# Kernel tuning notes

Measured on AMD Instinct MI355X. Metric: run time of the kernel, lower is better.

The kernel has to match this reference:

```python
import jax, jax.numpy as jnp
import numpy as np
import math

B, H, W, DM = 4, 64, 64, 96
DS, DCONV, EXPAND = 16, 3, 2
DI = EXPAND * DM
DTR = math.ceil(DM / 16)
K = 4
HID = 4 * DI


def layernorm(x, g, b, eps=1e-5):
    m = x.mean(-1, keepdims=True)
    v = ((x - m) ** 2).mean(-1, keepdims=True)
    return (x - m) / jnp.sqrt(v + eps) * g + b


def dwconv(x, w, b=None):
    # x: (B,C,H,W), w: (C,1,kh,kw) depthwise, odd kernel => SAME padding == k//2
    out = jax.lax.conv_general_dilated(x, w, (1, 1), 'SAME',
                                       feature_group_count=x.shape[1],
                                       dimension_numbers=('NCHW', 'OIHW', 'NCHW'))
    if b is not None:
        out = out + b[None, :, None, None]
    return out


def ss2d_core(xc, x_proj_w, dt_projs_w, dt_projs_b, A_logs, Ds):
    # xc: (b, d_inner, h, w) -> (b, d_inner, L) summed over 4 scan directions
    b, c, h, w = xc.shape
    L = h * w
    x_hw = xc.reshape(b, c, L)
    x_wh = xc.transpose(0, 1, 3, 2).reshape(b, c, L)
    xs = jnp.stack([x_hw, x_wh], axis=1)                 # (b,2,c,L)
    xs = jnp.concatenate([xs, jnp.flip(xs, -1)], axis=1)  # (b,4,c,L)
    x_dbl = jnp.einsum('bkdl,kcd->bkcl', xs, x_proj_w)
    dts, Bs, Cs = jnp.split(x_dbl, [DTR, DTR + DS], axis=2)
    dts = jnp.einsum('bkrl,kdr->bkdl', dts, dt_projs_w)
    delta = jax.nn.softplus(dts + dt_projs_b[None, :, :, None])  # (b,K,c,L)
    A = -jnp.exp(A_logs).reshape(K, c, DS)                       # (K,c,n)

    def step(hst, inp):
        x_t, d_t, B_t, C_t = inp  # (b,K,c),(b,K,c),(b,K,n),(b,K,n)
        dA = jnp.exp(d_t[..., None] * A)                       # (b,K,c,n)
        hst = hst * dA + (d_t * x_t)[..., None] * B_t[:, :, None, :]
        y = jnp.einsum('bkdn,bkn->bkd', hst, C_t)
        return hst, y

    seq = (jnp.moveaxis(xs, -1, 0), jnp.moveaxis(delta, -1, 0),
           jnp.moveaxis(Bs, -1, 0), jnp.moveaxis(Cs, -1, 0))
    h0 = jnp.zeros((b, K, c, DS), xc.dtype)
    _, ys = jax.lax.scan(step, h0, seq)          # (L,b,K,c)
    ys = jnp.moveaxis(ys, 0, -1)                 # (b,K,c,L)
    ys = ys + Ds.reshape(K, c)[None, :, :, None] * xs
    y1 = ys[:, 0]
    inv = jnp.flip(ys[:, 2:4], -1)
    y2 = inv[:, 0]
    wh = ys[:, 1].reshape(b, c, w, h).swapaxes(2, 3).reshape(b, c, L)
    invwh = inv[:, 1].reshape(b, c, w, h).swapaxes(2, 3).reshape(b, c, L)
    return y1 + y2 + wh + invwh


def msffn(y, in_w, in_b, dw1, dw3, dw5, ln_g, ln_b, out_w, out_b):
    hcl = jax.nn.silu(y @ in_w.T + in_b)          # (b,h,w,HID)
    hc = hcl.transpose(0, 3, 1, 2)
    hc = hc + dwconv(hc, dw1) + dwconv(hc, dw3) + dwconv(hc, dw5)
    hn = layernorm(hc.transpose(0, 2, 3, 1), ln_g, ln_b)
    return hn @ out_w.T + out_b


def setup_inputs() -> dict:
    key = jax.random.key(0)
    ks = jax.random.split(key, 16)
    dt_init_std = DTR ** -0.5
    dt = jnp.exp(jax.random.uniform(ks[0], (K, DI)) * (math.log(0.1) - math.log(0.001)) + math.log(0.001))
    dt = jnp.clip(dt, 1e-4, None)
    inv_dt = dt + jnp.log(-jnp.expm1(-dt))          # softplus-inverse init for dt bias
    A_logs = jnp.tile(jnp.log(jnp.arange(1, DS + 1, dtype=jnp.float32))[None, :], (K * DI, 1))
    r = lambda i, sh, s: jax.random.normal(ks[i], sh, jnp.float32) * s
    return {
        'x': r(1, (B, H, W, DM), 1.0),
        'in_proj_w': r(2, (2 * DI, DM), DM ** -0.5),
        'conv_w': r(3, (DI, 1, DCONV, DCONV), 0.2),
        'conv_b': jnp.zeros((DI,), jnp.float32),
        'x_proj_w': r(4, (K, DTR + 2 * DS, DI), DI ** -0.5),
        'dt_projs_w': jax.random.uniform(ks[5], (K, DI, DTR), minval=-dt_init_std, maxval=dt_init_std),
        'dt_projs_b': inv_dt,
        'A_logs': A_logs,
        'Ds': jnp.ones((K * DI,), jnp.float32),
        'out_norm_g': jnp.ones((DI,), jnp.float32),
        'out_norm_b': jnp.zeros((DI,), jnp.float32),
        'out_proj_w': r(6, (DM, DI), DI ** -0.5),
        'ffn_in_w': r(7, (HID, DI), DI ** -0.5),
        'ffn_in_b': jnp.zeros((HID,), jnp.float32),
        'ffn_dw1': r(8, (HID, 1, 1, 1), 0.3),
        'ffn_dw3': r(9, (HID, 1, 3, 3), 0.2),
        'ffn_dw5': r(10, (HID, 1, 5, 5), 0.1),
        'ffn_ln_g': jnp.ones((HID,), jnp.float32),
        'ffn_ln_b': jnp.zeros((HID,), jnp.float32),
        'ffn_out_w': r(11, (DM, HID), HID ** -0.5),
        'ffn_out_b': jnp.zeros((DM,), jnp.float32),
        'skip_scale': jnp.ones((1,), jnp.float32),
    }


def reference(x, in_proj_w, conv_w, conv_b, x_proj_w, dt_projs_w, dt_projs_b, A_logs, Ds,
              out_norm_g, out_norm_b, out_proj_w, ffn_in_w, ffn_in_b, ffn_dw1, ffn_dw3,
              ffn_dw5, ffn_ln_g, ffn_ln_b, ffn_out_w, ffn_out_b, skip_scale):
    b, h, w, _ = x.shape
    xz = x @ in_proj_w.T                          # (b,h,w,2*DI)
    xi, z = jnp.split(xz, 2, axis=-1)
    xc = jax.nn.silu(dwconv(xi.transpose(0, 3, 1, 2), conv_w, conv_b))  # (b,DI,h,w)
    y = ss2d_core(xc, x_proj_w, dt_projs_w, dt_projs_b, A_logs, Ds)     # (b,DI,L)
    y = y.swapaxes(1, 2).reshape(b, h, w, DI)
    y = layernorm(y, out_norm_g, out_norm_b)
    y = y * jax.nn.silu(z)
    out = y @ out_proj_w.T
    ffn = msffn(y, ffn_in_w, ffn_in_b, ffn_dw1, ffn_dw3, ffn_dw5,
                ffn_ln_g, ffn_ln_b, ffn_out_w, ffn_out_b)
    return out + skip_scale * ffn
```

## Files before the change

kernel.cpp:

```cpp
#include <hip/hip_runtime.h>
#include <hip/hip_bf16.h>

constexpr int BB = 4, HH = 64, WW = 64, DMv = 96;
constexpr int DSn = 16, DIv = 192, DTRv = 6, KKv = 4, HIDv = 768;
constexpr int LL = 4096;
constexpr int NC = 32, CHK = LL / NC;
constexpr int NR = BB * LL;
constexpr int XDS = 40;

constexpr size_t S_xi   = (size_t)BB * LL * DIv;
constexpr size_t S_xdbl = (size_t)BB * KKv * LL * XDS;
constexpr size_t S_big  = (size_t)BB * KKv * LL * DIv;
constexpr size_t S_sp   = (size_t)BB * KKv * NC * DIv * DSn;

typedef __attribute__((ext_vector_type(8))) short short8;
typedef __attribute__((ext_vector_type(4))) short short4v;
typedef __attribute__((ext_vector_type(4))) float floatx4;

__device__ __forceinline__ float sigf(float x) { return 1.f / (1.f + __expf(-x)); }
__device__ __forceinline__ float softp(float x) {
  return (x > 20.f) ? x : __logf(1.f + __expf(x));
}
__device__ __forceinline__ short bfbits(float v) {
  __hip_bfloat16 h = __float2bfloat16(v);
  return *(short*)&h;
}

__device__ __forceinline__ int lmap(int k, int l) {
  int lr = (k & 2) ? (LL - 1 - l) : l;
  return (k & 1) ? (((lr & 63) << 6) | (lr >> 6)) : lr;
}

__global__ void k_wprep(const float* __restrict__ fiw, const float* __restrict__ opw,
                        const float* __restrict__ fow, const float* __restrict__ in_w,
                        const float* __restrict__ xpw, const float* __restrict__ x,
                        float* __restrict__ wt, float* __restrict__ wcatT,
                        float* __restrict__ xt, short* __restrict__ fiwP,
                        short* __restrict__ opwP, short* __restrict__ fowP) {
  int bx = blockIdx.x, t = threadIdx.x;
  __shared__ float smbuf[32 * 65];
  if (bx < 36) {
    int r0 = (bx / 3) * 32, c0 = (bx % 3) * 32;
    float (*tile)[33] = (float(*)[33])smbuf;
    int tc = t & 31, tr = t >> 5;
#pragma unroll
    for (int i = 0; i < 4; ++i)
      tile[tr + i * 8][tc] = in_w[(size_t)(r0 + tr + i * 8) * 96 + c0 + tc];
    __syncthreads();
#pragma unroll
    for (int i = 0; i < 4; ++i)
      wt[(size_t)(c0 + tr + i * 8) * 384 + r0 + tc] = tile[tc][tr + i * 8];
    return;
  }
  if (bx < 150) {
    int idx = (bx - 36) * 256 + t;
    if (idx < 2 * 192 * 76) {
      int p = idx / (192 * 76);
      int rem = idx % (192 * 76);
      int d = rem / 76, j = rem % 76;
      int k = (j >= 38 ? 2 : 0) + p;
      int c = (j >= 38) ? j - 38 : j;
      wcatT[idx] = xpw[((size_t)(k * 38 + c)) * DIv + d];
    }
    return;
  }
  if (bx < 918) {
    int i4 = bx - 150;
    int r0 = (i4 / 3) * 64, k0 = (i4 % 3) * 32;
    float (*tile)[65] = (float(*)[65])smbuf;
#pragma unroll
    for (int ii = 0; ii < 8; ++ii) {
      int i = (t >> 5) + ii * 8, j = t & 31;
      tile[j][i] = x[(size_t)(r0 + i) * 96 + k0 + j];
    }
    __syncthreads();
#pragma unroll
    for (int jj = 0; jj < 8; ++jj) {
      int j = (t >> 6) + jj * 4, i = t & 63;
      xt[(size_t)(k0 + j) * NR + r0 + i] = tile[j][i];
    }
    return;
  }
  int lane = t & 63, ln16 = lane & 15, qd = lane >> 4;
  if (bx < 990) {
    int f = (bx - 918) * 4 + (t >> 6);
    int kt = f / 48, ntg = f % 48;
    int n = ntg * 16 + ln16;
#pragma unroll
    for (int j = 0; j < 8; ++j) {
      int k = kt * 32 + qd * 8 + j;
      fiwP[(size_t)f * 512 + lane * 8 + j] = bfbits(fiw[(size_t)n * DIv + k]);
    }
    return;
  }
  if (bx < 1008) {
    int u = (bx - 990) * 4 + (t >> 6);
    int f = u >> 1, part = u & 1;
    int kt = f / 6, ntg = f % 6;
    int n = ntg * 16 + ln16;
#pragma unroll
    for (int j = 0; j < 8; ++j) {
      int k = kt * 32 + qd * 8 + j;
      float w = opw[(size_t)n * DIv + k];
      __hip_bfloat16 h = __float2bfloat16(w);
      float v = part ? (w - (float)h) : w;
      opwP[((size_t)(part * 36 + f)) * 512 + lane * 8 + j] = bfbits(v);
    }
    return;
  }
  {
    int u = (bx - 1008) * 4 + (t >> 6);
    int f = u >> 1, part = u & 1;
    int kt = f / 6, ntg = f % 6;
    int n = ntg * 16 + ln16;
#pragma unroll
    for (int j = 0; j < 8; ++j) {
      int k = kt * 32 + qd * 8 + j;
      float w = fow[(size_t)n * HIDv + k];
      __hip_bfloat16 h = __float2bfloat16(w);
      float v = part ? (w - (float)h) : w;
      fowP[((size_t)(part * 144 + f)) * 512 + lane * 8 + j] = bfbits(v);
    }
  }
}

__global__ void k_inproj(const float* __restrict__ xt, const float* __restrict__ wt,
                         float* __restrict__ xi, float* __restrict__ z) {
  int t = threadIdx.x;
  int wv = t >> 6, lane = t & 63;
  int rq = blockIdx.x * 256 + wv * 64 + lane;
  int c0 = blockIdx.y * 8;
  const float4* xt4 = (const float4*)xt;
  float4 acc[8];
#pragma unroll
  for (int c = 0; c < 8; ++c) acc[c] = make_float4(0.f, 0.f, 0.f, 0.f);
  for (int k = 0; k < 96; ++k) {
    float4 xv = xt4[(size_t)k * (NR / 4) + rq];
    const float* wr = wt + k * 384 + c0;
#pragma unroll
    for (int c = 0; c < 8; ++c) {
      float w = wr[c];
      acc[c].x += w * xv.x; acc[c].y += w * xv.y;
      acc[c].z += w * xv.z; acc[c].w += w * xv.w;
    }
  }
  float* dst; int cc;
  if (c0 < DIv) { dst = xi; cc = c0; } else { dst = z; cc = c0 - DIv; }
#pragma unroll
  for (int li = 0; li < 4; ++li) {
    size_t row = (size_t)rq * 4 + li;
    float4 v0, v1;
    v0.x = (&acc[0].x)[li]; v0.y = (&acc[1].x)[li];
    v0.z = (&acc[2].x)[li]; v0.w = (&acc[3].x)[li];
    v1.x = (&acc[4].x)[li]; v1.y = (&acc[5].x)[li];
    v1.z = (&acc[6].x)[li]; v1.w = (&acc[7].x)[li];
    float4* o4 = (float4*)(dst + row * DIv + cc);
    o4[0] = v0; o4[1] = v1;
  }
}

constexpr int TW2 = 18;
__global__ void k_dwconv3(const float* __restrict__ xi, const float* __restrict__ cw,
                          const float* __restrict__ cb, float* __restrict__ xc,
                          float* __restrict__ xcT, float* __restrict__ xcTs) {
  int tile = blockIdx.x;
  int cg = blockIdx.y, b = blockIdx.z;
  int t = threadIdx.x;
  int ti0 = (tile >> 2) * 16, tj0 = (tile & 3) * 16;
  __shared__ float sm[TW2 * TW2 * 32];

  for (int e = t; e < TW2 * TW2 * 32; e += 256) {
    int ec = e & 31;
    int sp = e >> 5;
    int hi = sp / TW2, hj = sp % TW2;
    int gi = ti0 + hi - 1, gj = tj0 + hj - 1;
    float v = 0.f;
    if ((unsigned)gi < (unsigned)HH && (unsigned)gj < (unsigned)WW)
      v = xi[((size_t)b * LL + gi * WW + gj) * DIv + cg * 32 + ec];
    sm[e] = v;
  }

  int c = t & 31, s0 = t >> 5;
  int cglob = cg * 32 + c;
  float wc[9];
#pragma unroll
  for (int j = 0; j < 9; ++j) wc[j] = cw[cglob * 9 + j];
  float bv = cb[cglob];
  __syncthreads();

  float res[32];
  for (int i = 0; i < 32; ++i) {
    int p = s0 + (i << 3);
    int r = p >> 4, q = p & 15;
    float s = bv;
#pragma unroll
    for (int di = 0; di < 3; ++di)
#pragma unroll
      for (int dj = 0; dj < 3; ++dj)
        s += sm[((r + di) * TW2 + (q + dj)) * 32 + c] * wc[di * 3 + dj];
    res[i] = s * sigf(s);
  }
  __syncthreads();
  for (int i = 0; i < 32; ++i) {
    int p = s0 + (i << 3);
    sm[p * 35 + c] = res[i];
  }
  __syncthreads();
  for (int it = 0; it < 32; ++it) {
    int e = it * 256 + t;
    int p = e >> 5, ec = e & 31;
    int l = (ti0 + (p >> 4)) * WW + tj0 + (p & 15);
    xc[((size_t)b * LL + l) * DIv + cg * 32 + ec] = sm[p * 35 + ec];
  }
  for (int d2 = 0; d2 < 32; ++d2) {
    int l = (ti0 + (t >> 4)) * WW + tj0 + (t & 15);
    xcT[(size_t)(cg * 32 + d2) * NR + b * LL + l] = sm[t * 35 + d2];
  }
  for (int d2 = 0; d2 < 32; ++d2) {
    int gjo = t >> 4, gio = t & 15;
    int lt2 = (tj0 + gjo) * WW + ti0 + gio;
    int p = gio * 16 + gjo;
    xcTs[(size_t)(cg * 32 + d2) * NR + b * LL + lt2] = sm[p * 35 + d2];
  }
}

__global__ void k_xdbl2(const float* __restrict__ xcT, const float* __restrict__ xcTs,
                        const float* __restrict__ wcatT, float* __restrict__ xdbl) {
  int t = threadIdx.x;
  int rq = blockIdx.x * 256 + t;
  int jg = blockIdx.y;
  int pb = blockIdx.z;
  int p = pb >> 2, b = pb & 3;
  const float4* A = (const float4*)(p ? xcTs : xcT);
  const float* wbase = wcatT + (size_t)p * 192 * 76 + jg * 4;
  float4 acc[4];
#pragma unroll
  for (int j = 0; j < 4; ++j) acc[j] = make_float4(0.f, 0.f, 0.f, 0.f);
  for (int d = 0; d < 192; ++d) {
    float4 xv = A[(size_t)d * (NR / 4) + b * 1024 + rq];
    const float* wr = wbase + d * 76;
#pragma unroll
    for (int j = 0; j < 4; ++j) {
      float w = wr[j];
      acc[j].x += w * xv.x; acc[j].y += w * xv.y;
      acc[j].z += w * xv.z; acc[j].w += w * xv.w;
    }
  }
#pragma unroll
  for (int li = 0; li < 4; ++li) {
    int r = rq * 4 + li;
#pragma unroll
    for (int j = 0; j < 4; ++j) {
      int col = jg * 4 + j;
      int kk = (col >= 38) ? (2 + p) : p;
      int c = (col >= 38) ? col - 38 : col;
      int l = (col >= 38) ? (LL - 1 - r) : r;
      int phys = c + (c >= 6 ? 2 : 0);
      size_t ro = (((size_t)(b * KKv + kk)) * LL + l) * XDS;
      xdbl[ro + phys] = (&acc[j].x)[li];
      if (col == 5) { xdbl[ro + 6] = 0.f; xdbl[ro + 7] = 0.f; }
    }
  }
}

__global__ void k_scan1(const float* __restrict__ xdbl, const float* __restrict__ xc,
                        const float* __restrict__ alogs, const float* __restrict__ dtw,
                        const float* __restrict__ dtb,
                        float* __restrict__ S, float* __restrict__ P) {
  int bx = blockIdx.x;
  int c = bx / 3, dblk = bx % 3;
  int k = blockIdx.y, b = blockIdx.z;
  int t = threadIdx.x, dl = t >> 2, nq = t & 3;
  int d = dblk * 64 + dl;
  __shared__ float de_s[16][64], xv_s[16][64], bc_s[16][32], dt_s[16][8];
  float A[4];
#pragma unroll
  for (int j = 0; j < 4; ++j)
    A[j] = -__expf(alogs[(size_t)(k * DIv + d) * DSn + nq * 4 + j]);
  int derow = t >> 4, dec0 = (t & 15) * 4;
  float DTW[4][6], DTB[4];
#pragma unroll
  for (int jj = 0; jj < 4; ++jj) {
    int dd = k * DIv + dblk * 64 + dec0 + jj;
    DTB[jj] = dtb[dd];
#pragma unroll
    for (int r2 = 0; r2 < 6; ++r2) DTW[jj][r2] = dtw[(size_t)dd * 6 + r2];
  }
  size_t bkL = (size_t)(b * KKv + k) * LL;
  const float* xq = xdbl + bkL * XDS;
  const float* xcb = xc + (size_t)b * LL * DIv;
  float h[4] = {0.f, 0.f, 0.f, 0.f}, sA[4] = {0.f, 0.f, 0.f, 0.f};
  int l0 = c * CHK;
  for (int tile = 0; tile < CHK / 16; ++tile) {
    int lt = l0 + tile * 16;
    __syncthreads();
    {
      int r = t >> 4, q = t & 15;
      int lc = lmap(k, lt + r);
      *(float4*)&xv_s[r][q * 4] = *(const float4*)(xcb + (size_t)lc * DIv + dblk * 64 + q * 4);
      if (t < 128) {
        int r2 = t >> 3, q2 = t & 7;
        *(float4*)&bc_s[r2][q2 * 4] = *(const float4*)(xq + (size_t)(lt + r2) * XDS + 8 + q2 * 4);
      } else if (t < 160) {
        int i3 = t - 128, r3 = i3 >> 1, half = i3 & 1;
        *(float4*)&dt_s[r3][half * 4] = *(const float4*)(xq + (size_t)(lt + r3) * XDS + half * 4);
      }
    }
    __syncthreads();
    {
#pragma unroll
      for (int jj = 0; jj < 4; ++jj) {
        float s = DTB[jj];
#pragma unroll
        for (int r2 = 0; r2 < 6; ++r2) s += dt_s[derow][r2] * DTW[jj][r2];
        de_s[derow][dec0 + jj] = softp(s);
      }
    }
    __syncthreads();
#pragma unroll
    for (int i2 = 0; i2 < 16; ++i2) {
      float de = de_s[i2][dl];
      float xv = xv_s[i2][dl];
      float4 Bv = *(float4*)&bc_s[i2][nq * 4];
      float db = de * xv;
#pragma unroll
      for (int j = 0; j < 4; ++j) {
        float u = de * A[j];
        sA[j] += u;
        h[j] = h[j] * __expf(u) + db * (&Bv.x)[j];
      }
    }
  }
  size_t o = ((((size_t)(b * KKv + k) * NC + c) * 3 + dblk) * 1024) + (size_t)t * 4;
  float4 hs, ps;
#pragma unroll
  for (int j = 0; j < 4; ++j) { (&hs.x)[j] = h[j]; (&ps.x)[j] = __expf(sA[j]); }
  *(float4*)(S + o) = hs;
  *(float4*)(P + o) = ps;
}

__global__ void k_scan2(float* __restrict__ S, const float* __restrict__ P) {
  int dblk = blockIdx.x, k = blockIdx.y, b = blockIdx.z;
  int t = threadIdx.x;
  size_t base = (((size_t)(b * KKv + k) * NC) * 3 + dblk) * 1024 + (size_t)t * 4;
  float4 h = make_float4(0.f, 0.f, 0.f, 0.f);
  for (int c = 0; c < NC; ++c) {
    size_t o = base + (size_t)c * 3 * 1024;
    float4 s = *(float4*)(S + o), p = *(float4*)(P + o);
    *(float4*)(S + o) = h;
    h.x = s.x + p.x * h.x; h.y = s.y + p.y * h.y;
    h.z = s.z + p.z * h.z; h.w = s.w + p.w * h.w;
  }
}

__global__ void k_scan3(const float* __restrict__ xdbl, const float* __restrict__ xc,
                        const float* __restrict__ alogs, const float* __restrict__ dtw,
                        const float* __restrict__ dtb,
                        const float* __restrict__ Hin, float* __restrict__ ys) {
  int bx = blockIdx.x;
  int c = bx / 3, dblk = bx % 3;
  int k = blockIdx.y, b = blockIdx.z;
  int t = threadIdx.x, dl = t >> 2, nq = t & 3;
  int d = dblk * 64 + dl;
  __shared__ float de_s[16][64], xv_s[16][64], bc_s[16][32], dt_s[16][8];
  float A[4];
#pragma unroll
  for (int j = 0; j < 4; ++j)
    A[j] = -__expf(alogs[(size_t)(k * DIv + d) * DSn + nq * 4 + j]);
  int derow = t >> 4, dec0 = (t & 15) * 4;
  float DTW[4][6], DTB[4];
#pragma unroll
  for (int jj = 0; jj < 4; ++jj) {
    int dd = k * DIv + dblk * 64 + dec0 + jj;
    DTB[jj] = dtb[dd];
#pragma unroll
    for (int r2 = 0; r2 < 6; ++r2) DTW[jj][r2] = dtw[(size_t)dd * 6 + r2];
  }
  size_t bkL = (size_t)(b * KKv + k) * LL;
  const float* xq = xdbl + bkL * XDS;
  const float* xcb = xc + (size_t)b * LL * DIv;
  float* yp = ys + bkL * DIv + d;
  size_t o = ((((size_t)(b * KKv + k) * NC + c) * 3 + dblk) * 1024) + (size_t)t * 4;
  float4 h4 = *(const float4*)(Hin + o);
  float h[4] = {h4.x, h4.y, h4.z, h4.w};
  int l0 = c * CHK;
  for (int tile = 0; tile < CHK / 16; ++tile) {
    int lt = l0 + tile * 16;
    __syncthreads();
    {
      int r = t >> 4, q = t & 15;
      int lc = lmap(k, lt + r);
      *(float4*)&xv_s[r][q * 4] = *(const float4*)(xcb + (size_t)lc * DIv + dblk * 64 + q * 4);
      if (t < 128) {
        int r2 = t >> 3, q2 = t & 7;
        *(float4*)&bc_s[r2][q2 * 4] = *(const float4*)(xq + (size_t)(lt + r2) * XDS + 8 + q2 * 4);
      } else if (t < 160) {
        int i3 = t - 128, r3 = i3 >> 1, half = i3 & 1;
        *(float4*)&dt_s[r3][half * 4] = *(const float4*)(xq + (size_t)(lt + r3) * XDS + half * 4);
      }
    }
    __syncthreads();
    {
#pragma unroll
      for (int jj = 0; jj < 4; ++jj) {
        float s = DTB[jj];
#pragma unroll
        for (int r2 = 0; r2 < 6; ++r2) s += dt_s[derow][r2] * DTW[jj][r2];
        de_s[derow][dec0 + jj] = softp(s);
      }
    }
    __syncthreads();
#pragma unroll
    for (int i2 = 0; i2 < 16; ++i2) {
      float de = de_s[i2][dl];
      float xv = xv_s[i2][dl];
      float4 Bv = *(float4*)&bc_s[i2][nq * 4];
      float4 Cv = *(float4*)&bc_s[i2][16 + nq * 4];
      float db = de * xv;
      float p = 0.f;
#pragma unroll
      for (int j = 0; j < 4; ++j) {
        h[j] = h[j] * __expf(de * A[j]) + db * (&Bv.x)[j];
        p += h[j] * (&Cv.x)[j];
      }
      p += __shfl_down(p, 2, 4);
      p += __shfl_down(p, 1, 4);
      if (nq == 0) yp[(size_t)(lt + i2) * DIv] = p;
    }
  }
}

__global__ void k_comlnt(const float* __restrict__ ys, const float* __restrict__ xc,
                         const float* __restrict__ Ds, const float* __restrict__ z,
                         const float* __restrict__ g, const float* __restrict__ be,
                         __hip_bfloat16* __restrict__ ygtB,
                         __hip_bfloat16* __restrict__ ygtBl) {
  int bl0 = blockIdx.x * 32;
  int b = bl0 >> 12, l0 = bl0 & 4095;
  int t = threadIdx.x;
  __shared__ float vbuf[32 * 193];
  __shared__ float m_[32], rs_[32];
  {
    int grp = t >> 6, lane6 = t & 63;
    size_t base = (size_t)b * KKv * LL * DIv;
#pragma unroll
    for (int i8 = 0; i8 < 8; ++i8) {
      int li = grp + i8 * 4;
      int l = l0 + li;
      int lT = ((l & 63) << 6) | (l >> 6);
      const float* r0 = ys + base + (size_t)l * DIv;
      const float* r2 = ys + base + ((size_t)2 * LL + (LL - 1 - l)) * DIv;
      const float* r1 = ys + base + ((size_t)1 * LL + lT) * DIv;
      const float* r3 = ys + base + ((size_t)3 * LL + (LL - 1 - lT)) * DIv;
      const float* xr = xc + ((size_t)b * LL + l) * DIv;
#pragma unroll
      for (int cc = 0; cc < 3; ++cc) {
        int d = lane6 + cc * 64;
        float sd = Ds[d] + Ds[DIv + d] + Ds[2 * DIv + d] + Ds[3 * DIv + d];
        vbuf[li * 193 + d] = r0[d] + r2[d] + r1[d] + r3[d] + sd * xr[d];
      }
    }
  }
  __syncthreads();
  {
    int r = t >> 3, q = t & 7;
    float s = 0.f, qq = 0.f;
#pragma unroll
    for (int j = 0; j < 24; ++j) {
      float v = vbuf[r * 193 + q + j * 8];
      s += v; qq += v * v;
    }
    s += __shfl_down(s, 4, 8); qq += __shfl_down(qq, 4, 8);
    s += __shfl_down(s, 2, 8); qq += __shfl_down(qq, 2, 8);
    s += __shfl_down(s, 1, 8); qq += __shfl_down(qq, 1, 8);
    if (q == 0) {
      float m = s / DIv;
      m_[r] = m;
      rs_[r] = rsqrtf(qq / DIv - m * m + 1e-5f);
    }
  }
  __syncthreads();
  int tc = t & 31, tr = t >> 5;
#pragma unroll
  for (int ch = 0; ch < 6; ++ch) {
    int c0 = ch * 32;
    float gg = g[c0 + tc], bb = be[c0 + tc];
#pragma unroll
    for (int i = 0; i < 4; ++i) {
      int r = tr + i * 8;
      float v = vbuf[r * 193 + c0 + tc];
      float zz = z[(size_t)(bl0 + r) * DIv + c0 + tc];
      float val = (v - m_[r]) * rs_[r] * gg + bb;
      float gated = val * zz * sigf(zz);
      __hip_bfloat16 h = __float2bfloat16(gated);
      ygtB[(size_t)(bl0 + r) * DIv + c0 + tc] = h;
      ygtBl[(size_t)(bl0 + r) * DIv + c0 + tc] = __float2bfloat16(gated - (float)h);
    }
  }
}

__global__ void k_ffnmf(const __hip_bfloat16* __restrict__ ygtB,
                        const short* __restrict__ fiwP,
                        const float* __restrict__ bias, float* __restrict__ hcl) {
  int t = threadIdx.x;
  int wv = t >> 6, lane = t & 63;
  int ln16 = lane & 15, qd = lane >> 4;
  int m0 = blockIdx.x * 64 + wv * 16;
  int n0 = blockIdx.y * 64;
  int ntg0 = n0 >> 4;
  floatx4 acc[4];
  floatx4 zero4 = {0.f, 0.f, 0.f, 0.f};
#pragma unroll
  for (int nt = 0; nt < 4; ++nt) acc[nt] = zero4;
  const short* arow = (const short*)ygtB + (size_t)(m0 + ln16) * DIv + qd * 8;
#pragma unroll
  for (int kt = 0; kt < 6; ++kt) {
    short8 a = *(const short8*)(arow + kt * 32);
    const short* bb = fiwP + ((size_t)(kt * 48 + ntg0) * 64 + lane) * 8;
#pragma unroll
    for (int nt = 0; nt < 4; ++nt) {
      short8 bfr = *(const short8*)(bb + (size_t)nt * 512);
      acc[nt] = __builtin_amdgcn_mfma_f32_16x16x32_bf16(a, bfr, acc[nt], 0, 0, 0);
    }
  }
#pragma unroll
  for (int nt = 0; nt < 4; ++nt) {
    int col = n0 + nt * 16 + ln16;
    float bv = bias[col];
#pragma unroll
    for (int r = 0; r < 4; ++r) {
      int row = m0 + qd * 4 + r;
      float s = acc[nt][r] + bv;
      hcl[(size_t)row * HIDv + col] = s * sigf(s);
    }
  }
}

constexpr int TS = 16, CG = 32, TW = TS + 4;
__global__ void k_ffnconv2(const float* __restrict__ hcl, const float* __restrict__ w1,
                           const float* __restrict__ w3, const float* __restrict__ w5,
                           float* __restrict__ hc2) {
  int tile = blockIdx.x;
  int cg = blockIdx.y, b = blockIdx.z;
  int t = threadIdx.x;
  int ti0 = (tile >> 2) * TS, tj0 = (tile & 3) * TS;
  __shared__ float sm[TW * TW * CG];

  for (int e = t; e < TW * TW * CG; e += 256) {
    int ec = e & 31;
    int sp = e >> 5;
    int hi = sp / TW, hj = sp % TW;
    int gi = ti0 + hi - 2, gj = tj0 + hj - 2;
    float v = 0.f;
    if ((unsigned)gi < (unsigned)HH && (unsigned)gj < (unsigned)WW)
      v = hcl[((size_t)b * LL + gi * WW + gj) * HIDv + cg * CG + ec];
    sm[e] = v;
  }

  int c = t & 31;
  int cglob = cg * CG + c;
  float wc[25];
#pragma unroll
  for (int di = 0; di < 5; ++di)
#pragma unroll
    for (int dj = 0; dj < 5; ++dj) {
      float w = w5[cglob * 25 + di * 5 + dj];
      if (di >= 1 && di <= 3 && dj >= 1 && dj <= 3)
        w += w3[cglob * 9 + (di - 1) * 3 + (dj - 1)];
      if (di == 2 && dj == 2) w += 1.f + w1[cglob];
      wc[di * 5 + dj] = w;
    }
  __syncthreads();

  int q2 = t >> 5;
#pragma unroll
  for (int half = 0; half < 2; ++half) {
    int q = q2 + half * 8;
    float win[5][5];
#pragma unroll
    for (int di = 0; di < 4; ++di)
#pragma unroll
      for (int dj = 0; dj < 5; ++dj)
        win[di][dj] = sm[(di * TW + (q + dj)) * CG + c];
#pragma unroll
    for (int r = 0; r < 16; ++r) {
      int slot = (r + 4) % 5;
#pragma unroll
      for (int dj = 0; dj < 5; ++dj)
        win[slot][dj] = sm[(((r + 4) * TW) + (q + dj)) * CG + c];
      float s = 0.f;
#pragma unroll
      for (int di = 0; di < 5; ++di) {
        int wsl = (r + di) % 5;
#pragma unroll
        for (int dj = 0; dj < 5; ++dj)
          s += win[wsl][dj] * wc[di * 5 + dj];
      }
      hc2[((size_t)b * LL + (ti0 + r) * WW + (tj0 + q)) * HIDv + cglob] = s;
    }
  }
}

constexpr int LNROWS = 16, LNPAD = 776;
__global__ void k_ln2b(const float* __restrict__ hc2, const float* __restrict__ g,
                       const float* __restrict__ be,
                       short* __restrict__ hnBh, short* __restrict__ hnBl) {
  int r0 = blockIdx.x * LNROWS;
  int t = threadIdx.x;
  __shared__ float rows[LNROWS * LNPAD];
  __shared__ float m_[LNROWS], rs_[LNROWS];
#pragma unroll
  for (int i = 0; i < 12; ++i) {
    int idx4 = t + i * 256;
    int row = idx4 / 192, c4 = idx4 % 192;
    float4 v = *(const float4*)(hc2 + (size_t)(r0 + row) * HIDv + c4 * 4);
    *(float4*)&rows[row * LNPAD + c4 * 4] = v;
  }
  __syncthreads();
  {
    int r = t >> 4, q = t & 15;
    float s = 0.f, qq = 0.f;
#pragma unroll
    for (int j = 0; j < 48; ++j) {
      float v = rows[r * LNPAD + q + j * 16];
      s += v; qq += v * v;
    }
    s += __shfl_down(s, 8, 16); qq += __shfl_down(qq, 8, 16);
    s += __shfl_down(s, 4, 16); qq += __shfl_down(qq, 4, 16);
    s += __shfl_down(s, 2, 16); qq += __shfl_down(qq, 2, 16);
    s += __shfl_down(s, 1, 16); qq += __shfl_down(qq, 1, 16);
    if (q == 0) {
      float m = s / HIDv;
      m_[r] = m;
      rs_[r] = rsqrtf(qq / HIDv - m * m + 1e-5f);
    }
  }
  __syncthreads();
#pragma unroll
  for (int i = 0; i < 12; ++i) {
    int idx4 = t + i * 256;
    int row = idx4 / 192, c4 = idx4 % 192;
    float4 v = *(const float4*)&rows[row * LNPAD + c4 * 4];
    float4 gv = *(const float4*)(g + c4 * 4);
    float4 bv = *(const float4*)(be + c4 * 4);
    float m = m_[row], rs = rs_[row];
    short4v hh, ll;
#pragma unroll
    for (int j = 0; j < 4; ++j) {
      float val = ((&v.x)[j] - m) * rs * (&gv.x)[j] + (&bv.x)[j];
      __hip_bfloat16 h = __float2bfloat16(val);
      hh[j] = *(short*)&h;
      ll[j] = bfbits(val - (float)h);
    }
    size_t o = (size_t)(r0 + row) * HIDv + c4 * 4;
    *(short4v*)(hnBh + o) = hh;
    *(short4v*)(hnBl + o) = ll;
  }
}

__global__ void k_finalmf(const short* __restrict__ hnBh, const short* __restrict__ hnBl,
                          const short* __restrict__ fowP,
                          const short* __restrict__ ygtBh, const short* __restrict__ ygtBl,
                          const short* __restrict__ opwP,
                          const float* __restrict__ fob, const float* __restrict__ skip,
                          float* __restrict__ dout) {
  int t = threadIdx.x;
  int wv = t >> 6, lane = t & 63;
  int ln16 = lane & 15, qd = lane >> 4;
  int m0 = blockIdx.x * 64 + wv * 16;
  int ntg0 = blockIdx.y * 3;
  floatx4 accF[3], accO[3];
  floatx4 zero4 = {0.f, 0.f, 0.f, 0.f};
#pragma unroll
  for (int nt = 0; nt < 3; ++nt) { accF[nt] = zero4; accO[nt] = zero4; }
  const short* arh = hnBh + (size_t)(m0 + ln16) * HIDv + qd * 8;
  const short* arl = hnBl + (size_t)(m0 + ln16) * HIDv + qd * 8;
#pragma unroll 4
  for (int kt = 0; kt < 24; ++kt) {
    short8 ah = *(const short8*)(arh + kt * 32);
    short8 al = *(const short8*)(arl + kt * 32);
    const short* bh = fowP + ((size_t)(kt * 6 + ntg0) * 64 + lane) * 8;
    const short* bl = fowP + ((size_t)(144 + kt * 6 + ntg0) * 64 + lane) * 8;
#pragma unroll
    for (int nt = 0; nt < 3; ++nt) {
      short8 bhv = *(const short8*)(bh + (size_t)nt * 512);
      short8 blv = *(const short8*)(bl + (size_t)nt * 512);
      accF[nt] = __builtin_amdgcn_mfma_f32_16x16x32_bf16(ah, bhv, accF[nt], 0, 0, 0);
      accF[nt] = __builtin_amdgcn_mfma_f32_16x16x32_bf16(al, bhv, accF[nt], 0, 0, 0);
      accF[nt] = __builtin_amdgcn_mfma_f32_16x16x32_bf16(ah, blv, accF[nt], 0, 0, 0);
    }
  }
  const short* orh = ygtBh + (size_t)(m0 + ln16) * DIv + qd * 8;
  const short* orl = ygtBl + (size_t)(m0 + ln16) * DIv + qd * 8;
#pragma unroll
  for (int kt = 0; kt < 6; ++kt) {
    short8 ah = *(const short8*)(orh + kt * 32);
    short8 al = *(const short8*)(orl + kt * 32);
    const short* bh = opwP + ((size_t)(kt * 6 + ntg0) * 64 + lane) * 8;
    const short* bl = opwP + ((size_t)(36 + kt * 6 + ntg0) * 64 + lane) * 8;
#pragma unroll
    for (int nt = 0; nt < 3; ++nt) {
      short8 bhv = *(const short8*)(bh + (size_t)nt * 512);
      short8 blv = *(const short8*)(bl + (size_t)nt * 512);
      accO[nt] = __builtin_amdgcn_mfma_f32_16x16x32_bf16(ah, bhv, accO[nt], 0, 0, 0);
      accO[nt] = __builtin_amdgcn_mfma_f32_16x16x32_bf16(al, bhv, accO[nt], 0, 0, 0);
      accO[nt] = __builtin_amdgcn_mfma_f32_16x16x32_bf16(ah, blv, accO[nt], 0, 0, 0);
    }
  }
  float sk = skip[0];
#pragma unroll
  for (int nt = 0; nt < 3; ++nt) {
    int col = (ntg0 + nt) * 16 + ln16;
    float bv = fob[col];
#pragma unroll
    for (int r = 0; r < 4; ++r) {
      int row = m0 + qd * 4 + r;
      dout[(size_t)row * DMv + col] = accO[nt][r] + sk * (accF[nt][r] + bv);
    }
  }
}

extern "C" void kernel_launch(void* const* d_in, const int* in_sizes, int n_in,
                              void* d_out, int out_size, void* d_ws, size_t ws_size,
                              hipStream_t stream) {
  const float* x        = (const float*)d_in[0];
  const float* in_w     = (const float*)d_in[1];
  const float* conv_w   = (const float*)d_in[2];
  const float* conv_b   = (const float*)d_in[3];
  const float* xpw      = (const float*)d_in[4];
  const float* dtw      = (const float*)d_in[5];
  const float* dtb      = (const float*)d_in[6];
  const float* alogs    = (const float*)d_in[7];
  const float* Ds       = (const float*)d_in[8];
  const float* ong      = (const float*)d_in[9];
  const float* onb      = (const float*)d_in[10];
  const float* opw      = (const float*)d_in[11];
  const float* fiw      = (const float*)d_in[12];
  const float* fib      = (const float*)d_in[13];
  const float* dw1      = (const float*)d_in[14];
  const float* dw3      = (const float*)d_in[15];
  const float* dw5      = (const float*)d_in[16];
  const float* flg      = (const float*)d_in[17];
  const float* flb      = (const float*)d_in[18];
  const float* fow      = (const float*)d_in[19];
  const float* fob      = (const float*)d_in[20];
  const float* skip     = (const float*)d_in[21];

  float* ws    = (float*)d_ws;
  float* xi    = ws;
  float* z     = xi + S_xi;
  float* xc    = z + S_xi;
  float* xdbl  = xc + S_xi;
  float* scr   = xdbl + S_xdbl;
  float* ys    = scr + S_big;
  float* wtiny = ys + S_big;
  float* wcatT = wtiny;
  float* wt    = wcatT + 29184;
  __hip_bfloat16* ygtB = (__hip_bfloat16*)(wt + 36864);
  short* fiwP  = (short*)(wt + 36864) + (size_t)NR * DIv;
  short* opwP  = fiwP + 288 * 512;
  short* fowP  = opwP + 2 * 36 * 512;

  float* xt = scr;
  k_wprep<<<1080, 256, 0, stream>>>(fiw, opw, fow, in_w, xpw, x,
                                    wt, wcatT, xt, fiwP, opwP, fowP);

  dim3 gip(NR / 1024, 48);
  k_inproj<<<gip, 256, 0, stream>>>(xt, wt, xi, z);

  float* xcT  = ys;
  float* xcTs = ys + S_xi;
  dim3 gdw(16, DIv / 32, BB);
  k_dwconv3<<<gdw, 256, 0, stream>>>(xi, conv_w, conv_b, xc, xcT, xcTs);

  dim3 gxd(4, 19, 8);
  k_xdbl2<<<gxd, 256, 0, stream>>>(xcT, xcTs, wcatT, xdbl);

  float* Sbuf = xi;
  float* Pbuf = xi + S_sp;
  dim3 gs13(NC * 3, KKv, BB);
  dim3 gs2(3, KKv, BB);
  k_scan1<<<gs13, 256, 0, stream>>>(xdbl, xc, alogs, dtw, dtb, Sbuf, Pbuf);
  k_scan2<<<gs2, 256, 0, stream>>>(Sbuf, Pbuf);
  k_scan3<<<gs13, 256, 0, stream>>>(xdbl, xc, alogs, dtw, dtb, Sbuf, ys);

  __hip_bfloat16* ygtBl = (__hip_bfloat16*)xi;
  k_comlnt<<<NR / 32, 256, 0, stream>>>(ys, xc, Ds, z, ong, onb, ygtB, ygtBl);

  float* hcl = scr;
  dim3 gmf(NR / 64, HIDv / 64);
  k_ffnmf<<<gmf, 256, 0, stream>>>(ygtB, fiwP, fib, hcl);

  float* hc2 = ys;
  dim3 gc(16, HIDv / CG, BB);
  k_ffnconv2<<<gc, 256, 0, stream>>>(hcl, dw1, dw3, dw5, hc2);

  short* hnBh = (short*)scr;
  short* hnBl = hnBh + (size_t)NR * HIDv;
  k_ln2b<<<NR / LNROWS, 256, 0, stream>>>(hc2, flg, flb, hnBh, hnBl);

  dim3 gfm(NR / 64, 2);
  k_finalmf<<<gfm, 256, 0, stream>>>(hnBh, hnBl, fowP,
                                     (const short*)ygtB, (const short*)ygtBl, opwP,
                                     fob, skip, (float*)d_out);
}
```

Before: 430.9 us.

## Double scan chunk count and compute delta directly from global dt loads

Raises the number of chunks in the chunked selective scan from 32 to 64, halving chunk length and doubling the blocks in scan1/scan3. This gives more parallelism while making the serial chunk-combine pass in scan2 longer. Each thread now reads its six dt values straight from global memory instead of staging them in shared memory, which removes one barrier per tile. scan1 also loads only the B columns it needs. The S/P state buffers move to the scr scratch area because they are now twice as large, which risks overlapping other live data.

```diff
diff --git a/kernel.cpp b/kernel.cpp
--- a/kernel.cpp
+++ b/kernel.cpp
@@ -4,7 +4,7 @@
 constexpr int BB = 4, HH = 64, WW = 64, DMv = 96;
 constexpr int DSn = 16, DIv = 192, DTRv = 6, KKv = 4, HIDv = 768;
 constexpr int LL = 4096;
-constexpr int NC = 32, CHK = LL / NC;
+constexpr int NC = 64, CHK = LL / NC;
 constexpr int NR = BB * LL;
 constexpr int XDS = 40;
 
@@ -272,7 +272,7 @@
   int k = blockIdx.y, b = blockIdx.z;
   int t = threadIdx.x, dl = t >> 2, nq = t & 3;
   int d = dblk * 64 + dl;
-  __shared__ float de_s[16][64], xv_s[16][64], bc_s[16][32], dt_s[16][8];
+  __shared__ float de_s[16][64], xv_s[16][64], bc_s[16][16];
   float A[4];
 #pragma unroll
   for (int j = 0; j < 4; ++j)
@@ -298,21 +298,16 @@
       int r = t >> 4, q = t & 15;
       int lc = lmap(k, lt + r);
       *(float4*)&xv_s[r][q * 4] = *(const float4*)(xcb + (size_t)lc * DIv + dblk * 64 + q * 4);
-      if (t < 128) {
-        int r2 = t >> 3, q2 = t & 7;
+      if (t < 64) {
+        int r2 = t >> 2, q2 = t & 3;
         *(float4*)&bc_s[r2][q2 * 4] = *(const float4*)(xq + (size_t)(lt + r2) * XDS + 8 + q2 * 4);
-      } else if (t < 160) {
-        int i3 = t - 128, r3 = i3 >> 1, half = i3 & 1;
-        *(float4*)&dt_s[r3][half * 4] = *(const float4*)(xq + (size_t)(lt + r3) * XDS + half * 4);
       }
-    }
-    __syncthreads();
-    {
+      const float* dtp = xq + (size_t)(lt + derow) * XDS;
+      float d0 = dtp[0], d1 = dtp[1], d2 = dtp[2], d3 = dtp[3], d4 = dtp[4], d5 = dtp[5];
 #pragma unroll
       for (int jj = 0; jj < 4; ++jj) {
-        float s = DTB[jj];
-#pragma unroll
-        for (int r2 = 0; r2 < 6; ++r2) s += dt_s[derow][r2] * DTW[jj][r2];
+        float s = DTB[jj] + d0 * DTW[jj][0] + d1 * DTW[jj][1] + d2 * DTW[jj][2]
+                          + d3 * DTW[jj][3] + d4 * DTW[jj][4] + d5 * DTW[jj][5];
         de_s[derow][dec0 + jj] = softp(s);
       }
     }
@@ -362,7 +357,7 @@
   int k = blockIdx.y, b = blockIdx.z;
   int t = threadIdx.x, dl = t >> 2, nq = t & 3;
   int d = dblk * 64 + dl;
-  __shared__ float de_s[16][64], xv_s[16][64], bc_s[16][32], dt_s[16][8];
+  __shared__ float de_s[16][64], xv_s[16][64], bc_s[16][32];
   float A[4];
 #pragma unroll
   for (int j = 0; j < 4; ++j)
@@ -394,18 +389,13 @@
       if (t < 128) {
         int r2 = t >> 3, q2 = t & 7;
         *(float4*)&bc_s[r2][q2 * 4] = *(const float4*)(xq + (size_t)(lt + r2) * XDS + 8 + q2 * 4);
-      } else if (t < 160) {
-        int i3 = t - 128, r3 = i3 >> 1, half = i3 & 1;
-        *(float4*)&dt_s[r3][half * 4] = *(const float4*)(xq + (size_t)(lt + r3) * XDS + half * 4);
       }
-    }
-    __syncthreads();
-    {
+      const float* dtp = xq + (size_t)(lt + derow) * XDS;
+      float d0 = dtp[0], d1 = dtp[1], d2 = dtp[2], d3 = dtp[3], d4 = dtp[4], d5 = dtp[5];
 #pragma unroll
       for (int jj = 0; jj < 4; ++jj) {
-        float s = DTB[jj];
-#pragma unroll
-        for (int r2 = 0; r2 < 6; ++r2) s += dt_s[derow][r2] * DTW[jj][r2];
+        float s = DTB[jj] + d0 * DTW[jj][0] + d1 * DTW[jj][1] + d2 * DTW[jj][2]
+                          + d3 * DTW[jj][3] + d4 * DTW[jj][4] + d5 * DTW[jj][5];
         de_s[derow][dec0 + jj] = softp(s);
       }
     }
@@ -776,8 +766,8 @@
   dim3 gxd(4, 19, 8);
   k_xdbl2<<<gxd, 256, 0, stream>>>(xcT, xcTs, wcatT, xdbl);
 
-  float* Sbuf = xi;
-  float* Pbuf = xi + S_sp;
+  float* Sbuf = scr;
+  float* Pbuf = scr + S_sp;
   dim3 gs13(NC * 3, KKv, BB);
   dim3 gs2(3, KKv, BB);
   k_scan1<<<gs13, 256, 0, stream>>>(xdbl, xc, alogs, dtw, dtb, Sbuf, Pbuf);
```

New measurement: 433.5 us. Within noise of the previous version (+0.6%).
